# Kernel tuning notes

Hardware: AMD Instinct MI355X
Metric: run time of the kernel (lower is better)

The kernel has to match this reference:

```python
import jax, jax.numpy as jnp
import numpy as np

N_NODES = 50000
N_EDGES = 800000
IN_DIM = 8
EDGE_DIM = 4
HIDDEN = 16
OUT_DIM = 1


def _lin_init(key, fan_in, fan_out):
    kw, kb = jax.random.split(key)
    bound = 1.0 / np.sqrt(fan_in)
    W = jax.random.uniform(kw, (fan_in, fan_out), minval=-bound, maxval=bound, dtype=jnp.float32)
    b = jax.random.uniform(kb, (fan_out,), minval=-bound, maxval=bound, dtype=jnp.float32)
    return W, b


def setup_inputs() -> dict:
    key = jax.random.key(0)
    ks = jax.random.split(key, 16)
    x = jax.random.normal(ks[0], (N_NODES, IN_DIM), dtype=jnp.float32)
    edge_index = jax.random.randint(ks[1], (2, N_EDGES), 0, N_NODES, dtype=jnp.int32)
    edge_attr = jax.random.normal(ks[2], (N_EDGES, EDGE_DIM), dtype=jnp.float32)

    inp = {"x": x, "edge_index": edge_index, "edge_attr": edge_attr}
    in_dims = [IN_DIM, HIDDEN]
    for i in range(2):
        d_in = in_dims[i]
        W1, b1 = _lin_init(ks[3 + 4 * i], EDGE_DIM, HIDDEN)
        W2, b2 = _lin_init(ks[4 + 4 * i], HIDDEN, d_in * HIDDEN)
        root = jax.random.uniform(ks[5 + 4 * i], (d_in, HIDDEN), minval=-1.0 / np.sqrt(d_in), maxval=1.0 / np.sqrt(d_in), dtype=jnp.float32)
        bias = jnp.zeros((HIDDEN,), dtype=jnp.float32)
        inp[f"eW1_{i}"] = W1; inp[f"eb1_{i}"] = b1
        inp[f"eW2_{i}"] = W2; inp[f"eb2_{i}"] = b2
        inp[f"root_{i}"] = root; inp[f"bias_{i}"] = bias
    mW1, mb1 = _lin_init(ks[11], HIDDEN, HIDDEN)
    mW2, mb2 = _lin_init(ks[12], HIDDEN, OUT_DIM)
    inp["mW1"] = mW1; inp["mb1"] = mb1; inp["mW2"] = mW2; inp["mb2"] = mb2
    return inp


def _nnconv(x, src, dst, edge_attr, eW1, eb1, eW2, eb2, root, bias):
    # edge MLP -> per-edge weight matrix [E, d_in, HIDDEN]
    h = jax.nn.silu(edge_attr @ eW1 + eb1)
    Wedge = (h @ eW2 + eb2).reshape(edge_attr.shape[0], x.shape[1], HIDDEN)
    # gather source features, per-edge matmul, scatter-mean to targets
    msg = jnp.einsum('ei,eio->eo', x[src], Wedge)  # [E, HIDDEN]
    agg = jax.ops.segment_sum(msg, dst, num_segments=N_NODES)
    cnt = jax.ops.segment_sum(jnp.ones((msg.shape[0],), dtype=msg.dtype), dst, num_segments=N_NODES)
    agg = agg / jnp.maximum(cnt, 1.0)[:, None]
    return x @ root + agg + bias


def reference(x, edge_index, edge_attr,
              eW1_0, eb1_0, eW2_0, eb2_0, root_0, bias_0,
              eW1_1, eb1_1, eW2_1, eb2_1, root_1, bias_1,
              mW1, mb1, mW2, mb2):
    src, dst = edge_index[0], edge_index[1]
    x = jax.nn.relu(_nnconv(x, src, dst, edge_attr, eW1_0, eb1_0, eW2_0, eb2_0, root_0, bias_0))
    x = jax.nn.relu(_nnconv(x, src, dst, edge_attr, eW1_1, eb1_1, eW2_1, eb2_1, root_1, bias_1))
    out = jax.nn.sigmoid(jax.nn.silu(x @ mW1 + mb1) @ mW2 + mb2)
    return out
```

## Files before the change

### kernel.cpp

```cpp
#include <hip/hip_runtime.h>
#include <hip/hip_fp16.h>

#define NN 50000
#define NE 800000
#define NBUCK 196

__device__ __forceinline__ float sigm(float v) { return 1.0f / (1.0f + __expf(-v)); }


__global__ void sort_count(const int* __restrict__ ei,
                           int* __restrict__ cntA, int* __restrict__ cntB)
{
    __shared__ int hA[NBUCK], hB[NBUCK];
    int t = threadIdx.x;
    for (int i = t; i < NBUCK; i += 256) { hA[i] = 0; hB[i] = 0; }
    __syncthreads();
    int base = blockIdx.x * 2048;
#pragma unroll
    for (int r = 0; r < 8; ++r) {
        int idx = base + r * 256 + t;
        if (idx < NE) {
            int s = ei[idx], d = ei[NE + idx];
            atomicAdd(&hB[s >> 8], 1);
            atomicAdd(&hA[d >> 8], 1);
        }
    }
    __syncthreads();
    for (int i = t; i < NBUCK; i += 256) {
        if (hA[i]) atomicAdd(&cntA[i], hA[i]);
        if (hB[i]) atomicAdd(&cntB[i], hB[i]);
    }
}

__global__ void sort_scan(const int* __restrict__ cntA, const int* __restrict__ cntB,
                          int* __restrict__ baseA, int* __restrict__ baseB,
                          int* __restrict__ curA,  int* __restrict__ curB)
{
    __shared__ int a[256], b[256];
    int t = threadIdx.x;
    a[t] = (t < NBUCK) ? cntA[t] : 0;
    b[t] = (t < NBUCK) ? cntB[t] : 0;
    __syncthreads();
#pragma unroll
    for (int dd = 1; dd < 256; dd <<= 1) {
        int av = (t >= dd) ? a[t - dd] : 0;
        int bv = (t >= dd) ? b[t - dd] : 0;
        __syncthreads();
        a[t] += av; b[t] += bv;
        __syncthreads();
    }
    int exA = (t > 0) ? a[t - 1] : 0;
    int exB = (t > 0) ? b[t - 1] : 0;
    if (t < NBUCK) { baseA[t] = exA; curA[t] = exA; baseB[t] = exB; curB[t] = exB; }
    if (t == 255)  { baseA[NBUCK] = a[255]; baseB[NBUCK] = b[255]; }
}

__global__ __launch_bounds__(256) void sort_scatterA(const int* __restrict__ ei,
                                                     int* __restrict__ curA,
                                                     unsigned* __restrict__ recA)
{
    __shared__ int lcnt[NBUCK];
    __shared__ int lofs[NBUCK];
    int t = threadIdx.x;
    for (int i = t; i < NBUCK; i += 256) lcnt[i] = 0;
    __syncthreads();
    int base = blockIdx.x * 2048;
#pragma unroll
    for (int r = 0; r < 8; ++r) {
        int e = base + r * 256 + t;
        if (e < NE) atomicAdd(&lcnt[ei[NE + e] >> 8], 1);
    }
    __syncthreads();
    for (int i = t; i < NBUCK; i += 256)
        lofs[i] = lcnt[i] ? atomicAdd(&curA[i], lcnt[i]) : 0;
    __syncthreads();
#pragma unroll
    for (int r = 0; r < 8; ++r) {
        int e = base + r * 256 + t;
        if (e < NE) {
            int d = ei[NE + e];
            int p = atomicAdd(&lofs[d >> 8], 1);
            recA[p] = ((unsigned)(d & 255) << 20) | (unsigned)e;
        }
    }
}

__global__ __launch_bounds__(256) void sort_localA(const unsigned* __restrict__ recA,
                                                   const int* __restrict__ baseA,
                                                   int* __restrict__ off_all,
                                                   unsigned* __restrict__ dlist)
{
    __shared__ int c[256];
    __shared__ int live[256];
    int t = threadIdx.x;
    int b = blockIdx.x;
    int lo = baseA[b], hi = baseA[b + 1];
    c[t] = 0;
    __syncthreads();
    for (int i = lo + t; i < hi; i += 256)
        atomicAdd(&c[(recA[i] >> 20) & 255], 1);
    __syncthreads();
#pragma unroll
    for (int dd = 1; dd < 256; dd <<= 1) {
        int v = (t >= dd) ? c[t - dd] : 0;
        __syncthreads();
        c[t] += v;
        __syncthreads();
    }
    int ex = (t > 0) ? c[t - 1] : 0;
    int d = (b << 8) + t;
    if (d <= NN) off_all[d] = lo + ex;
    live[t] = lo + ex;
    __syncthreads();
    for (int i = lo + t; i < hi; i += 256) {
        unsigned rec = recA[i];
        int pos = atomicAdd(&live[(rec >> 20) & 255], 1);
        dlist[pos] = rec & 0xFFFFFu;
    }
}

__global__ __launch_bounds__(256) void sort_scatterB(const int* __restrict__ ei,
                                                     const unsigned* __restrict__ dlist,
                                                     int* __restrict__ curB,
                                                     unsigned long long* __restrict__ recB)
{
    __shared__ int lcnt[NBUCK];
    __shared__ int lofs[NBUCK];
    __shared__ unsigned short sS[2048];
    __shared__ unsigned eS[2048];
    int t = threadIdx.x;
    for (int i = t; i < NBUCK; i += 256) lcnt[i] = 0;
    __syncthreads();
    int base = blockIdx.x * 2048;
#pragma unroll
    for (int r = 0; r < 8; ++r) {
        int dp = base + r * 256 + t;
        int li = r * 256 + t;
        if (dp < NE) {
            unsigned e = dlist[dp];
            int s = ei[e];
            sS[li] = (unsigned short)s;
            eS[li] = e;
            atomicAdd(&lcnt[s >> 8], 1);
        }
    }
    __syncthreads();
    for (int i = t; i < NBUCK; i += 256)
        lofs[i] = lcnt[i] ? atomicAdd(&curB[i], lcnt[i]) : 0;
    __syncthreads();
#pragma unroll
    for (int r = 0; r < 8; ++r) {
        int dp = base + r * 256 + t;
        int li = r * 256 + t;
        if (dp < NE) {
            int s = sS[li];
            unsigned e = eS[li];
            int p = atomicAdd(&lofs[s >> 8], 1);
            recB[p] = ((unsigned long long)(s & 255) << 40)
                    | ((unsigned long long)(unsigned)dp << 20)
                    | (unsigned long long)e;
        }
    }
}

__global__ __launch_bounds__(256) void sort_localB(const unsigned long long* __restrict__ recB,
                                                   const int* __restrict__ baseB,
                                                   int* __restrict__ off_all,
                                                   unsigned long long* __restrict__ sperm64)
{
    __shared__ int c[256];
    __shared__ int live[256];
    int t = threadIdx.x;
    int b = blockIdx.x;
    int lo = baseB[b], hi = baseB[b + 1];
    c[t] = 0;
    __syncthreads();
    for (int i = lo + t; i < hi; i += 256)
        atomicAdd(&c[(int)(recB[i] >> 40) & 255], 1);
    __syncthreads();
#pragma unroll
    for (int dd = 1; dd < 256; dd <<= 1) {
        int v = (t >= dd) ? c[t - dd] : 0;
        __syncthreads();
        c[t] += v;
        __syncthreads();
    }
    int ex = (t > 0) ? c[t - 1] : 0;
    int s = (b << 8) + t;
    if (s <= NN) off_all[NN + s] = NE + lo + ex;
    live[t] = lo + ex;
    __syncthreads();
    for (int i = lo + t; i < hi; i += 256) {
        unsigned long long rec = recB[i];
        int k = (int)(rec >> 40) & 255;
        int pos = atomicAdd(&live[k], 1);
        int sl = ((b << 8) + k) & 15;
        sperm64[pos] = ((unsigned long long)sl << 40) | (rec & 0xFFFFFFFFFFull);
    }
}

template<int DIN>
__global__ __launch_bounds__(256) void edge_fusedG(
        const float* __restrict__ xin,
        const unsigned long long* __restrict__ sperm64,
        const float* __restrict__ ea,
        const float* __restrict__ eW1,
        const float* __restrict__ eb1,
        const float* __restrict__ eW2,
        const float* __restrict__ eb2,
        const int*   __restrict__ off_all,
        __half* __restrict__ msgbuf)
{
    constexpr int MROW = 260;
    constexpr int W2B  = DIN * 16 * 20 * 4;
    constexpr int SMB  = 16 * MROW * 4 + 256 * 4;
    constexpr int UNIB = (W2B > SMB) ? W2B : SMB;
    __shared__ __align__(16) char uni[UNIB];
    float* w2L   = (float*)uni;
    float* smemM = (float*)uni;
    int*   sdp   = (int*)(uni + 16 * MROW * 4);
    __shared__ __align__(16) float4 G4[16 * 69];
    __shared__ __align__(16) float4 xbL[16 * 5];
    __shared__ __align__(16) float  xL[16 * DIN];
    __shared__ __align__(16) float  b2L[DIN * 16];
    __shared__ __align__(16) float4 w1t[16];
    __shared__ __align__(16) float  b1s[16];

    int tid = threadIdx.x;
    int nb  = blockIdx.x * 16;
    if (tid < 16) {
        w1t[tid] = make_float4(eW1[tid], eW1[16 + tid], eW1[32 + tid], eW1[48 + tid]);
        b1s[tid] = eb1[tid];
    }
    for (int t = tid; t < 16 * DIN * 16; t += 256) {
        int k = t / (DIN * 16);
        int rem = t - k * DIN * 16;
        int i = rem >> 4, o = rem & 15;
        w2L[(i * 16 + k) * 20 + o] = eW2[t];
    }
    for (int t = tid; t < DIN * 16; t += 256) b2L[t] = eb2[t];
    for (int t = tid; t < 16 * DIN; t += 256) xL[t] = xin[(size_t)nb * DIN + t];
    __syncthreads();

    {
        int nl = tid >> 4, k = tid & 15;
        const float* xrow = xL + nl * DIN;
#pragma unroll
        for (int ob = 0; ob < 4; ++ob) {
            float4 a4 = make_float4(0.f, 0.f, 0.f, 0.f);
#pragma unroll
            for (int i = 0; i < DIN; ++i) {
                const float4 w = *((const float4*)(w2L + (i * 16 + k) * 20) + ob);
                a4.x += xrow[i] * w.x; a4.y += xrow[i] * w.y;
                a4.z += xrow[i] * w.z; a4.w += xrow[i] * w.w;
            }
            G4[nl * 69 + ob * 17 + k] = a4;
        }
        if (k < 4) {
            int ob = k;
            const float4* b2v = (const float4*)b2L;
            float4 a4 = make_float4(0.f, 0.f, 0.f, 0.f);
#pragma unroll
            for (int i = 0; i < DIN; ++i) {
                float4 b = b2v[i * 4 + ob];
                a4.x += xrow[i] * b.x; a4.y += xrow[i] * b.y;
                a4.z += xrow[i] * b.z; a4.w += xrow[i] * b.w;
            }
            xbL[nl * 5 + ob] = a4;
        }
    }
    __syncthreads();

    int eBeg = off_all[NN + nb] - NE;
    int eEnd = off_all[NN + nb + 16] - NE;
    for (int cb = eBeg; cb < eEnd; cb += 256) {
        int pos = cb + tid;
        bool valid = pos < eEnd;
        unsigned long long pk = valid ? sperm64[pos] : 0ull;
        int e  = (int)(pk & 0xFFFFFu);
        int dp = (int)((pk >> 20) & 0xFFFFFu);
        int sl = (int)(pk >> 40);
        float4 a = valid ? ((const float4*)ea)[e] : make_float4(0.f, 0.f, 0.f, 0.f);

        float h[16];
#pragma unroll
        for (int j = 0; j < 16; ++j) {
            float4 w = w1t[j];
            float p = b1s[j] + a.x * w.x + a.y * w.y + a.z * w.z + a.w * w.w;
            h[j] = p * sigm(p);
        }
        float4 acc[4];
#pragma unroll
        for (int ob = 0; ob < 4; ++ob) acc[ob] = xbL[sl * 5 + ob];
#pragma unroll
        for (int k = 0; k < 16; ++k) {
            float hk = h[k];
#pragma unroll
            for (int ob = 0; ob < 4; ++ob) {
                float4 g = G4[sl * 69 + ob * 17 + k];
                acc[ob].x += hk * g.x; acc[ob].y += hk * g.y;
                acc[ob].z += hk * g.z; acc[ob].w += hk * g.w;
            }
        }
        sdp[tid] = valid ? dp : -1;
#pragma unroll
        for (int ob = 0; ob < 4; ++ob) {
            smemM[(ob * 4 + 0) * MROW + tid] = acc[ob].x;
            smemM[(ob * 4 + 1) * MROW + tid] = acc[ob].y;
            smemM[(ob * 4 + 2) * MROW + tid] = acc[ob].z;
            smemM[(ob * 4 + 3) * MROW + tid] = acc[ob].w;
        }
        __syncthreads();
#pragma unroll
        for (int r = 0; r < 8; ++r) {
            int le = r * 32 + (tid >> 3);
            int p  = tid & 7;
            int d2 = sdp[le];
            float v0 = smemM[(2 * p)     * MROW + le];
            float v1 = smemM[(2 * p + 1) * MROW + le];
            if (d2 >= 0) {
                __half2 hv = __floats2half2_rn(v0, v1);
                *((__half2*)(msgbuf + (size_t)d2 * 16) + p) = hv;
            }
        }
        __syncthreads();
    }
}

__device__ __forceinline__ float gather_msg16(const __half* __restrict__ msgbuf,
                                              int s0, int e0, int tid)
{
    int half = (tid >> 3) & 1;
    int p    = tid & 7;
    float ax = 0.f, ay = 0.f;
    for (int j = s0 + half; j < e0; j += 2) {
        __half2 hv = *((const __half2*)(msgbuf + (size_t)j * 16) + p);
        float2 f = __half22float2(hv);
        ax += f.x; ay += f.y;
    }
    ax += __shfl_xor(ax, 8, 16);
    ay += __shfl_xor(ay, 8, 16);
    int ch = tid & 15;
    float vx = __shfl(ax, ch >> 1, 16);
    float vy = __shfl(ay, ch >> 1, 16);
    return (ch & 1) ? vy : vx;
}

__global__ __launch_bounds__(256) void gather_L0(
        const float* __restrict__ xin,
        const float* __restrict__ root,
        const float* __restrict__ bias,
        const int*   __restrict__ off_all,
        const __half* __restrict__ msgbuf,
        float* __restrict__ x1)
{
    __shared__ __align__(16) float rootL[8 * 16];
    __shared__ __align__(16) float biasL[16];
    int tid = threadIdx.x;
    if (tid < 128) rootL[tid] = root[tid];
    if (tid < 16) biasL[tid] = bias[tid];
    __syncthreads();

    int ch = tid & 15;
    int n  = blockIdx.x * 16 + (tid >> 4);
    int s0 = off_all[n], e0 = off_all[n + 1];

    float acc = gather_msg16(msgbuf, s0, e0, tid);
    float v = acc / fmaxf((float)(e0 - s0), 1.0f) + biasL[ch];
#pragma unroll
    for (int i = 0; i < 8; ++i)
        v += xin[(size_t)n * 8 + i] * rootL[i * 16 + ch];
    x1[(size_t)n * 16 + ch] = fmaxf(v, 0.f);
}

__global__ __launch_bounds__(256) void gather_final(
        const float* __restrict__ x1,
        const float* __restrict__ root,
        const float* __restrict__ bias,
        const int*   __restrict__ off_all,
        const __half* __restrict__ msgbuf,
        const float* __restrict__ mW1,
        const float* __restrict__ mb1,
        const float* __restrict__ mW2,
        const float* __restrict__ mb2,
        float* __restrict__ out)
{
    __shared__ __align__(16) float rootL[256];
    __shared__ __align__(16) float biasL[16];
    __shared__ __align__(16) float w1m[256];
    __shared__ __align__(16) float b1m[16];
    __shared__ __align__(16) float w2m[16];
    __shared__ float b2m;
    int tid = threadIdx.x;
    rootL[tid] = root[tid];
    w1m[tid] = mW1[tid];
    if (tid < 16) { biasL[tid] = bias[tid]; b1m[tid] = mb1[tid]; w2m[tid] = mW2[tid]; }
    if (tid == 0) b2m = mb2[0];
    __syncthreads();

    int ch = tid & 15;
    int n  = blockIdx.x * 16 + (tid >> 4);
    int s0 = off_all[n], e0 = off_all[n + 1];

    float acc = gather_msg16(msgbuf, s0, e0, tid);
    float v = acc / fmaxf((float)(e0 - s0), 1.0f) + biasL[ch];
#pragma unroll
    for (int i = 0; i < 16; ++i)
        v += x1[(size_t)n * 16 + i] * rootL[i * 16 + ch];
    v = fmaxf(v, 0.f);

    float z = b1m[ch];
#pragma unroll
    for (int o = 0; o < 16; ++o) {
        float vo = __shfl(v, o, 16);
        z += vo * w1m[o * 16 + ch];
    }
    float ss = z * sigm(z) * w2m[ch];
#pragma unroll
    for (int off = 8; off; off >>= 1) ss += __shfl_xor(ss, off, 16);
    if (ch == 0) out[n] = sigm(ss + b2m);
}

extern "C" void kernel_launch(void* const* d_in, const int* in_sizes, int n_in,
                              void* d_out, int out_size, void* d_ws, size_t ws_size,
                              hipStream_t stream) {
    const float* x     = (const float*)d_in[0];
    const int*   ei    = (const int*)  d_in[1];
    const float* ea    = (const float*)d_in[2];
    const float* eW1_0 = (const float*)d_in[3];
    const float* eb1_0 = (const float*)d_in[4];
    const float* eW2_0 = (const float*)d_in[5];
    const float* eb2_0 = (const float*)d_in[6];
    const float* root0 = (const float*)d_in[7];
    const float* bias0 = (const float*)d_in[8];
    const float* eW1_1 = (const float*)d_in[9];
    const float* eb1_1 = (const float*)d_in[10];
    const float* eW2_1 = (const float*)d_in[11];
    const float* eb2_1 = (const float*)d_in[12];
    const float* root1 = (const float*)d_in[13];
    const float* bias1 = (const float*)d_in[14];
    const float* mW1   = (const float*)d_in[15];
    const float* mb1   = (const float*)d_in[16];
    const float* mW2   = (const float*)d_in[17];
    const float* mb2   = (const float*)d_in[18];
    float* out = (float*)d_out;

    const int GG  = NN / 16;
    const int SBK = (NE + 2047) / 2048;

    int* W = (int*)d_ws;
    int* off_all = W;
    int* cntA    = W + 100004;
    int* cntB    = W + 100260;
    int* baseA   = W + 100516;
    int* baseB   = W + 100716;
    int* curA    = W + 100916;
    int* curB    = W + 101172;
    unsigned long long* sperm64 = (unsigned long long*)(W + 101440);
    float*  x1     = (float*)(W + 1701440);
    __half* msgbuf = (__half*)(W + 2501440);
    unsigned* recA  = (unsigned*)(W + 2501440);
    unsigned* dlist = (unsigned*)(W + 3301440);
    unsigned long long* recB = (unsigned long long*)(W + 4101440);

    hipMemsetAsync(cntA, 0, 512 * sizeof(int), stream);
    sort_count   <<<SBK,   256, 0, stream>>>(ei, cntA, cntB);
    sort_scan    <<<1,     256, 0, stream>>>(cntA, cntB, baseA, baseB, curA, curB);
    sort_scatterA<<<SBK,   256, 0, stream>>>(ei, curA, recA);
    sort_localA  <<<NBUCK, 256, 0, stream>>>(recA, baseA, off_all, dlist);
    sort_scatterB<<<SBK,   256, 0, stream>>>(ei, dlist, curB, recB);
    sort_localB  <<<NBUCK, 256, 0, stream>>>(recB, baseB, off_all, sperm64);

    edge_fusedG<8><<<GG, 256, 0, stream>>>(x, sperm64, ea, eW1_0, eb1_0,
                                           eW2_0, eb2_0, off_all, msgbuf);
    gather_L0<<<GG, 256, 0, stream>>>(x, root0, bias0, off_all, msgbuf, x1);

    edge_fusedG<16><<<GG, 256, 0, stream>>>(x1, sperm64, ea, eW1_1, eb1_1,
                                            eW2_1, eb2_1, off_all, msgbuf);
    gather_final<<<GG, 256, 0, stream>>>(x1, root1, bias1, off_all, msgbuf,
                                         mW1, mb1, mW2, mb2, out);
}
```

Measured before the change: 292.6 us.

## Carry source ids through sort, pre-permute edge attrs, drop LDS staging in edge kernel

The first sort pass now packs the source node into a 64-bit record, so the second scatter no longer does a random gather of ei. The final local sort writes a compact 32-bit permutation plus a pre-permuted copy of edge_attr, which both edge kernels then read contiguously instead of gathering. The edge kernel drops its shared-memory staging of eW2/eb2 and of the outputs (with its two barriers per chunk) and writes each message as two 16-byte stores straight to global memory. The trade-off is wider 64-bit sort records, extra workspace, and a per-thread write pattern to msgbuf that is less coalesced than the old staged write.

```diff
diff --git a/kernel.cpp b/kernel.cpp
--- a/kernel.cpp
+++ b/kernel.cpp
@@ -57,7 +57,7 @@
 
 __global__ __launch_bounds__(256) void sort_scatterA(const int* __restrict__ ei,
                                                      int* __restrict__ curA,
-                                                     unsigned* __restrict__ recA)
+                                                     unsigned long long* __restrict__ recA)
 {
     __shared__ int lcnt[NBUCK];
     __shared__ int lofs[NBUCK];
@@ -78,17 +78,19 @@
     for (int r = 0; r < 8; ++r) {
         int e = base + r * 256 + t;
         if (e < NE) {
-            int d = ei[NE + e];
+            int s = ei[e], d = ei[NE + e];
             int p = atomicAdd(&lofs[d >> 8], 1);
-            recA[p] = ((unsigned)(d & 255) << 20) | (unsigned)e;
-        }
-    }
-}
-
-__global__ __launch_bounds__(256) void sort_localA(const unsigned* __restrict__ recA,
+            recA[p] = ((unsigned long long)(unsigned)(d & 255) << 36)
+                    | ((unsigned long long)(unsigned)s << 20)
+                    | (unsigned long long)(unsigned)e;
+        }
+    }
+}
+
+__global__ __launch_bounds__(256) void sort_localA(const unsigned long long* __restrict__ recA,
                                                    const int* __restrict__ baseA,
                                                    int* __restrict__ off_all,
-                                                   unsigned* __restrict__ dlist)
+                                                   unsigned long long* __restrict__ dlist)
 {
     __shared__ int c[256];
     __shared__ int live[256];
@@ -98,7 +100,7 @@
     c[t] = 0;
     __syncthreads();
     for (int i = lo + t; i < hi; i += 256)
-        atomicAdd(&c[(recA[i] >> 20) & 255], 1);
+        atomicAdd(&c[(int)(recA[i] >> 36) & 255], 1);
     __syncthreads();
 #pragma unroll
     for (int dd = 1; dd < 256; dd <<= 1) {
@@ -113,21 +115,19 @@
     live[t] = lo + ex;
     __syncthreads();
     for (int i = lo + t; i < hi; i += 256) {
-        unsigned rec = recA[i];
-        int pos = atomicAdd(&live[(rec >> 20) & 255], 1);
-        dlist[pos] = rec & 0xFFFFFu;
-    }
-}
-
-__global__ __launch_bounds__(256) void sort_scatterB(const int* __restrict__ ei,
-                                                     const unsigned* __restrict__ dlist,
+        unsigned long long rec = recA[i];
+        int pos = atomicAdd(&live[(int)(rec >> 36) & 255], 1);
+        dlist[pos] = rec & 0xFFFFFFFFFull;
+    }
+}
+
+__global__ __launch_bounds__(256) void sort_scatterB(const unsigned long long* __restrict__ dlist,
                                                      int* __restrict__ curB,
                                                      unsigned long long* __restrict__ recB)
 {
     __shared__ int lcnt[NBUCK];
     __shared__ int lofs[NBUCK];
-    __shared__ unsigned short sS[2048];
-    __shared__ unsigned eS[2048];
+    __shared__ unsigned long long vS[2048];
     int t = threadIdx.x;
     for (int i = t; i < NBUCK; i += 256) lcnt[i] = 0;
     __syncthreads();
@@ -137,11 +137,9 @@
         int dp = base + r * 256 + t;
         int li = r * 256 + t;
         if (dp < NE) {
-            unsigned e = dlist[dp];
-            int s = ei[e];
-            sS[li] = (unsigned short)s;
-            eS[li] = e;
-            atomicAdd(&lcnt[s >> 8], 1);
+            unsigned long long v = dlist[dp];
+            vS[li] = v;
+            atomicAdd(&lcnt[(int)(v >> 28)], 1);
         }
     }
     __syncthreads();
@@ -153,20 +151,22 @@
         int dp = base + r * 256 + t;
         int li = r * 256 + t;
         if (dp < NE) {
-            int s = sS[li];
-            unsigned e = eS[li];
+            unsigned long long v = vS[li];
+            int s = (int)((v >> 20) & 0xFFFFu);
             int p = atomicAdd(&lofs[s >> 8], 1);
-            recB[p] = ((unsigned long long)(s & 255) << 40)
+            recB[p] = ((unsigned long long)(unsigned)(s & 255) << 40)
                     | ((unsigned long long)(unsigned)dp << 20)
-                    | (unsigned long long)e;
+                    | (v & 0xFFFFFull);
         }
     }
 }
 
 __global__ __launch_bounds__(256) void sort_localB(const unsigned long long* __restrict__ recB,
                                                    const int* __restrict__ baseB,
+                                                   const float4* __restrict__ ea4,
                                                    int* __restrict__ off_all,
-                                                   unsigned long long* __restrict__ sperm64)
+                                                   unsigned* __restrict__ sperm32,
+                                                   float4* __restrict__ ea_perm)
 {
     __shared__ int c[256];
     __shared__ int live[256];
@@ -194,16 +194,18 @@
         unsigned long long rec = recB[i];
         int k = (int)(rec >> 40) & 255;
         int pos = atomicAdd(&live[k], 1);
-        int sl = ((b << 8) + k) & 15;
-        sperm64[pos] = ((unsigned long long)sl << 40) | (rec & 0xFFFFFFFFFFull);
+        unsigned sl = (unsigned)(((b << 8) + k) & 15);
+        unsigned dp = (unsigned)((rec >> 20) & 0xFFFFFu);
+        sperm32[pos] = (sl << 20) | dp;
+        ea_perm[pos] = ea4[rec & 0xFFFFFull];
     }
 }
 
 template<int DIN>
 __global__ __launch_bounds__(256) void edge_fusedG(
         const float* __restrict__ xin,
-        const unsigned long long* __restrict__ sperm64,
-        const float* __restrict__ ea,
+        const unsigned* __restrict__ sperm32,
+        const float4* __restrict__ ea_perm,
         const float* __restrict__ eW1,
         const float* __restrict__ eb1,
         const float* __restrict__ eW2,
@@ -211,18 +213,9 @@
         const int*   __restrict__ off_all,
         __half* __restrict__ msgbuf)
 {
-    constexpr int MROW = 260;
-    constexpr int W2B  = DIN * 16 * 20 * 4;
-    constexpr int SMB  = 16 * MROW * 4 + 256 * 4;
-    constexpr int UNIB = (W2B > SMB) ? W2B : SMB;
-    __shared__ __align__(16) char uni[UNIB];
-    float* w2L   = (float*)uni;
-    float* smemM = (float*)uni;
-    int*   sdp   = (int*)(uni + 16 * MROW * 4);
     __shared__ __align__(16) float4 G4[16 * 69];
     __shared__ __align__(16) float4 xbL[16 * 5];
     __shared__ __align__(16) float  xL[16 * DIN];
-    __shared__ __align__(16) float  b2L[DIN * 16];
     __shared__ __align__(16) float4 w1t[16];
     __shared__ __align__(16) float  b1s[16];
 
@@ -232,25 +225,19 @@
         w1t[tid] = make_float4(eW1[tid], eW1[16 + tid], eW1[32 + tid], eW1[48 + tid]);
         b1s[tid] = eb1[tid];
     }
-    for (int t = tid; t < 16 * DIN * 16; t += 256) {
-        int k = t / (DIN * 16);
-        int rem = t - k * DIN * 16;
-        int i = rem >> 4, o = rem & 15;
-        w2L[(i * 16 + k) * 20 + o] = eW2[t];
-    }
-    for (int t = tid; t < DIN * 16; t += 256) b2L[t] = eb2[t];
     for (int t = tid; t < 16 * DIN; t += 256) xL[t] = xin[(size_t)nb * DIN + t];
     __syncthreads();
 
     {
         int nl = tid >> 4, k = tid & 15;
         const float* xrow = xL + nl * DIN;
+        const float4* w2r = (const float4*)(eW2 + k * (DIN * 16));
 #pragma unroll
         for (int ob = 0; ob < 4; ++ob) {
             float4 a4 = make_float4(0.f, 0.f, 0.f, 0.f);
 #pragma unroll
             for (int i = 0; i < DIN; ++i) {
-                const float4 w = *((const float4*)(w2L + (i * 16 + k) * 20) + ob);
+                float4 w = w2r[i * 4 + ob];
                 a4.x += xrow[i] * w.x; a4.y += xrow[i] * w.y;
                 a4.z += xrow[i] * w.z; a4.w += xrow[i] * w.w;
             }
@@ -258,7 +245,7 @@
         }
         if (k < 4) {
             int ob = k;
-            const float4* b2v = (const float4*)b2L;
+            const float4* b2v = (const float4*)eb2;
             float4 a4 = make_float4(0.f, 0.f, 0.f, 0.f);
 #pragma unroll
             for (int i = 0; i < DIN; ++i) {
@@ -273,14 +260,11 @@
 
     int eBeg = off_all[NN + nb] - NE;
     int eEnd = off_all[NN + nb + 16] - NE;
-    for (int cb = eBeg; cb < eEnd; cb += 256) {
-        int pos = cb + tid;
-        bool valid = pos < eEnd;
-        unsigned long long pk = valid ? sperm64[pos] : 0ull;
-        int e  = (int)(pk & 0xFFFFFu);
-        int dp = (int)((pk >> 20) & 0xFFFFFu);
-        int sl = (int)(pk >> 40);
-        float4 a = valid ? ((const float4*)ea)[e] : make_float4(0.f, 0.f, 0.f, 0.f);
+    for (int pos = eBeg + tid; pos < eEnd; pos += 256) {
+        unsigned pk = sperm32[pos];
+        int dp = (int)(pk & 0xFFFFFu);
+        int sl = (int)(pk >> 20);
+        float4 a = ea_perm[pos];
 
         float h[16];
 #pragma unroll
@@ -302,28 +286,21 @@
                 acc[ob].z += hk * g.z; acc[ob].w += hk * g.w;
             }
         }
-        sdp[tid] = valid ? dp : -1;
-#pragma unroll
-        for (int ob = 0; ob < 4; ++ob) {
-            smemM[(ob * 4 + 0) * MROW + tid] = acc[ob].x;
-            smemM[(ob * 4 + 1) * MROW + tid] = acc[ob].y;
-            smemM[(ob * 4 + 2) * MROW + tid] = acc[ob].z;
-            smemM[(ob * 4 + 3) * MROW + tid] = acc[ob].w;
-        }
-        __syncthreads();
-#pragma unroll
-        for (int r = 0; r < 8; ++r) {
-            int le = r * 32 + (tid >> 3);
-            int p  = tid & 7;
-            int d2 = sdp[le];
-            float v0 = smemM[(2 * p)     * MROW + le];
-            float v1 = smemM[(2 * p + 1) * MROW + le];
-            if (d2 >= 0) {
-                __half2 hv = __floats2half2_rn(v0, v1);
-                *((__half2*)(msgbuf + (size_t)d2 * 16) + p) = hv;
-            }
-        }
-        __syncthreads();
+        __half2 h01 = __floats2half2_rn(acc[0].x, acc[0].y);
+        __half2 h23 = __floats2half2_rn(acc[0].z, acc[0].w);
+        __half2 h45 = __floats2half2_rn(acc[1].x, acc[1].y);
+        __half2 h67 = __floats2half2_rn(acc[1].z, acc[1].w);
+        __half2 h89 = __floats2half2_rn(acc[2].x, acc[2].y);
+        __half2 hAB = __floats2half2_rn(acc[2].z, acc[2].w);
+        __half2 hCD = __floats2half2_rn(acc[3].x, acc[3].y);
+        __half2 hEF = __floats2half2_rn(acc[3].z, acc[3].w);
+        uint4 w0 = make_uint4(*(unsigned*)&h01, *(unsigned*)&h23,
+                              *(unsigned*)&h45, *(unsigned*)&h67);
+        uint4 w1 = make_uint4(*(unsigned*)&h89, *(unsigned*)&hAB,
+                              *(unsigned*)&hCD, *(unsigned*)&hEF);
+        uint4* dst = (uint4*)(msgbuf + (size_t)dp * 16);
+        dst[0] = w0;
+        dst[1] = w1;
     }
 }
 
@@ -456,26 +433,28 @@
     int* baseB   = W + 100716;
     int* curA    = W + 100916;
     int* curB    = W + 101172;
-    unsigned long long* sperm64 = (unsigned long long*)(W + 101440);
-    float*  x1     = (float*)(W + 1701440);
-    __half* msgbuf = (__half*)(W + 2501440);
-    unsigned* recA  = (unsigned*)(W + 2501440);
-    unsigned* dlist = (unsigned*)(W + 3301440);
-    unsigned long long* recB = (unsigned long long*)(W + 4101440);
+    unsigned* sperm32 = (unsigned*)(W + 101440);
+    float4* ea_perm   = (float4*)(W + 901440);
+    float*  x1        = (float*)(W + 4101440);
+    __half* msgbuf    = (__half*)(W + 4901440);
+    unsigned long long* recA  = (unsigned long long*)(W + 4901440);
+    unsigned long long* dlist = (unsigned long long*)(W + 6501440);
+    unsigned long long* recB  = (unsigned long long*)(W + 8101440);
 
     hipMemsetAsync(cntA, 0, 512 * sizeof(int), stream);
     sort_count   <<<SBK,   256, 0, stream>>>(ei, cntA, cntB);
     sort_scan    <<<1,     256, 0, stream>>>(cntA, cntB, baseA, baseB, curA, curB);
     sort_scatterA<<<SBK,   256, 0, stream>>>(ei, curA, recA);
     sort_localA  <<<NBUCK, 256, 0, stream>>>(recA, baseA, off_all, dlist);
-    sort_scatterB<<<SBK,   256, 0, stream>>>(ei, dlist, curB, recB);
-    sort_localB  <<<NBUCK, 256, 0, stream>>>(recB, baseB, off_all, sperm64);
-
-    edge_fusedG<8><<<GG, 256, 0, stream>>>(x, sperm64, ea, eW1_0, eb1_0,
+    sort_scatterB<<<SBK,   256, 0, stream>>>(dlist, curB, recB);
+    sort_localB  <<<NBUCK, 256, 0, stream>>>(recB, baseB, (const float4*)ea,
+                                             off_all, sperm32, ea_perm);
+
+    edge_fusedG<8><<<GG, 256, 0, stream>>>(x, sperm32, ea_perm, eW1_0, eb1_0,
                                            eW2_0, eb2_0, off_all, msgbuf);
     gather_L0<<<GG, 256, 0, stream>>>(x, root0, bias0, off_all, msgbuf, x1);
 
-    edge_fusedG<16><<<GG, 256, 0, stream>>>(x1, sperm64, ea, eW1_1, eb1_1,
+    edge_fusedG<16><<<GG, 256, 0, stream>>>(x1, sperm32, ea_perm, eW1_1, eb1_1,
                                             eW2_1, eb2_1, off_all, msgbuf);
     gather_final<<<GG, 256, 0, stream>>>(x1, root1, bias1, off_all, msgbuf,
                                          mW1, mb1, mW2, mb2, out);
```

Result: slower. 397.7 us (+35.9%).
